# Kernel tuning notes

Measured on AMD Instinct MI355X. Metric: run time of the kernel, lower is better.

Reference implementation:

```python
import jax, jax.numpy as jnp
import numpy as np

B, CH, N = 4, 128, 4096
PC = CH // 2  # pos channels = 64


def setup_inputs() -> dict:
    key = jax.random.key(0)
    ks = jax.random.split(key, 6)
    s_p = 1.0 / np.sqrt(PC)
    s_v = 1.0 / np.sqrt(CH)
    return {
        "pos_bot": jax.random.normal(ks[0], (B, PC, N), dtype=jnp.float32),
        "corr_feats": jax.random.normal(ks[1], (B, CH, N), dtype=jnp.float32),
        "Wp": jax.random.uniform(ks[2], (PC, PC), jnp.float32, -s_p, s_p),
        "bp": jax.random.uniform(ks[3], (PC,), jnp.float32, -s_p, s_p),
        "Wv": jax.random.uniform(ks[4], (CH, CH), jnp.float32, -s_v, s_v),
        "bv": jax.random.uniform(ks[5], (CH,), jnp.float32, -s_v, s_v),
        "beta": jnp.asarray([1.0], dtype=jnp.float32),
    }


def reference(pos_bot, corr_feats, Wp, bp, Wv, bv, beta):
    # 1x1 Conv1d == per-position matmul over channels
    pos = jnp.einsum("oc,bcn->bon", Wp, pos_bot) + bp[None, :, None]      # [B,64,N]
    value = jnp.einsum("oc,bcn->bon", Wv, corr_feats) + bv[None, :, None]  # [B,128,N]

    x = jnp.transpose(pos, (0, 2, 1))  # [B,N,64]
    # squared euclidean pairwise distance: ||xi||^2 + ||xj||^2 - 2 xi.xj
    sq = jnp.sum(x * x, axis=-1)  # [B,N]
    d2 = sq[:, :, None] + sq[:, None, :] - 2.0 * jnp.einsum("bnd,bmd->bnm", x, x)
    d2 = jnp.maximum(d2, 0.0)
    kernel = jnp.exp(-d2 * beta[0])  # [B,N,N] Gaussian RBF

    equation_F = jnp.transpose(value, (0, 2, 1))  # [B,N,128]
    return kernel, equation_F
```

## Files before the change

kernel.cpp:

```cpp
#include <hip/hip_runtime.h>
#include <hip/hip_bf16.h>

typedef _Float16 f16x8 __attribute__((ext_vector_type(8)));
typedef _Float16 f16x4 __attribute__((ext_vector_type(4)));
typedef float    f32x4 __attribute__((ext_vector_type(4)));

constexpr int BB = 4;
constexpr int CH = 128;
constexpr int PC = 64;
constexpr int NN = 4096;

__global__ __launch_bounds__(256) void proj_kernel(
    const float* __restrict__ pos_bot,
    const float* __restrict__ corr,
    const float* __restrict__ Wp,
    const float* __restrict__ bp,
    const float* __restrict__ Wv,
    const float* __restrict__ bv,
    _Float16* __restrict__ xbuf,
    float*    __restrict__ sq,
    float*    __restrict__ eqF)
{
    const int tid  = threadIdx.x;
    const int wid  = tid >> 6;
    const int lane = tid & 63;
    const int l15  = lane & 15;
    const int lg   = lane >> 4;
    const int b    = blockIdx.y & 3;
    const int n    = blockIdx.x * 16 + l15;

    if ((blockIdx.y >> 2) == 0) {
        const int mt = wid;
        f16x8 wf[2], pb[2];
#pragma unroll
        for (int ks = 0; ks < 2; ++ks) {
            const float* wp = Wp + (mt * 16 + l15) * PC + ks * 32 + lg * 8;
            f32x4 w0 = *reinterpret_cast<const f32x4*>(wp);
            f32x4 w1 = *reinterpret_cast<const f32x4*>(wp + 4);
            f16x8 f;
#pragma unroll
            for (int e = 0; e < 4; ++e) { f[e] = (_Float16)w0[e]; f[e + 4] = (_Float16)w1[e]; }
            wf[ks] = f;
            f16x8 g;
#pragma unroll
            for (int e = 0; e < 8; ++e) {
                const int c = ks * 32 + lg * 8 + e;
                g[e] = (_Float16)pos_bot[((size_t)(b * PC + c)) * NN + n];
            }
            pb[ks] = g;
        }

        f32x4 acc = {0.f, 0.f, 0.f, 0.f};
        acc = __builtin_amdgcn_mfma_f32_16x16x32_f16(wf[0], pb[0], acc, 0, 0, 0);
        acc = __builtin_amdgcn_mfma_f32_16x16x32_f16(wf[1], pb[1], acc, 0, 0, 0);

        float partial = 0.f;
        f16x4 h4;
#pragma unroll
        for (int r = 0; r < 4; ++r) {
            const int o = mt * 16 + lg * 4 + r;
            const float v = acc[r] + bp[o];
            const _Float16 h = (_Float16)v;
            h4[r] = h;
            const float hf = (float)h;
            partial = fmaf(hf, hf, partial);
        }
        *reinterpret_cast<f16x4*>(xbuf + ((size_t)(b * NN + n)) * PC + mt * 16 + lg * 4) = h4;

        partial += __shfl_xor(partial, 16);
        partial += __shfl_xor(partial, 32);
        __shared__ float psum[4][16];
        if (lane < 16) psum[wid][l15] = partial;
        __syncthreads();
        if (tid < 16)
            sq[b * NN + blockIdx.x * 16 + tid] =
                psum[0][tid] + psum[1][tid] + psum[2][tid] + psum[3][tid];
        return;
    }

    f16x8 cb[4];
#pragma unroll
    for (int ks = 0; ks < 4; ++ks) {
        f16x8 g;
#pragma unroll
        for (int e = 0; e < 8; ++e) {
            const int c = ks * 32 + lg * 8 + e;
            g[e] = (_Float16)corr[((size_t)(b * CH + c)) * NN + n];
        }
        cb[ks] = g;
    }
#pragma unroll
    for (int half = 0; half < 2; ++half) {
        const int ot = wid + half * 4;
        f32x4 acc = {0.f, 0.f, 0.f, 0.f};
#pragma unroll
        for (int ks = 0; ks < 4; ++ks) {
            const float* wv = Wv + (ot * 16 + l15) * CH + ks * 32 + lg * 8;
            f32x4 w0 = *reinterpret_cast<const f32x4*>(wv);
            f32x4 w1 = *reinterpret_cast<const f32x4*>(wv + 4);
            f16x8 f;
#pragma unroll
            for (int e = 0; e < 4; ++e) { f[e] = (_Float16)w0[e]; f[e + 4] = (_Float16)w1[e]; }
            acc = __builtin_amdgcn_mfma_f32_16x16x32_f16(f, cb[ks], acc, 0, 0, 0);
        }
        f32x4 o4;
#pragma unroll
        for (int r = 0; r < 4; ++r) o4[r] = acc[r] + bv[ot * 16 + lg * 4 + r];
        __builtin_nontemporal_store(
            o4, reinterpret_cast<f32x4*>(eqF + ((size_t)(b * NN + n)) * CH + ot * 16 + lg * 4));
    }
}

__global__ __launch_bounds__(256) void gram_kernel(
    const _Float16* __restrict__ xbuf,
    const float*    __restrict__ sq,
    const float*    __restrict__ beta,
    float*          __restrict__ out)
{
    const int tid  = threadIdx.x;
    const int wid  = tid >> 6;
    const int lane = tid & 63;
    const int l15  = lane & 15;
    const int lg   = lane >> 4;
    const int b    = blockIdx.z;
    const int jb   = blockIdx.x * 512;
    const int rb0  = blockIdx.y * 128;
    const int wjb  = jb + wid * 128;

    const _Float16* xb  = xbuf + (size_t)b * NN * PC;
    const float*    sqb = sq + (size_t)b * NN;

    const float bs   = -beta[0] * 1.44269504088896f;
    const float m2bs = -2.f * bs;

    f16x8 bf[8][2];
    float tj[8];
#pragma unroll
    for (int jtf = 0; jtf < 8; ++jtf) {
        const int j = wjb + jtf * 16 + l15;
#pragma unroll
        for (int ks = 0; ks < 2; ++ks)
            bf[jtf][ks] = *reinterpret_cast<const f16x8*>(
                xb + (size_t)j * PC + ks * 32 + lg * 8);
        tj[jtf] = bs * sqb[j];
    }

    __shared__ float lds[4][16][132];

    for (int rbh = 0; rbh < 2; ++rbh) {
        const int rb = rb0 + rbh * 64;

        for (int sl = 0; sl < 4; ++sl) {
            const int ibase = rb + sl * 16;

            const f16x8 af0 = *reinterpret_cast<const f16x8*>(
                xb + (size_t)(ibase + l15) * PC + lg * 8);
            const f16x8 af1 = *reinterpret_cast<const f16x8*>(
                xb + (size_t)(ibase + l15) * PC + 32 + lg * 8);

            f32x4 acc[8];
#pragma unroll
            for (int jtf = 0; jtf < 8; ++jtf) {
                f32x4 z = {0.f, 0.f, 0.f, 0.f};
                acc[jtf] = __builtin_amdgcn_mfma_f32_16x16x32_f16(af0, bf[jtf][0], z, 0, 0, 0);
            }
#pragma unroll
            for (int jtf = 0; jtf < 8; ++jtf)
                acc[jtf] = __builtin_amdgcn_mfma_f32_16x16x32_f16(af1, bf[jtf][1], acc[jtf], 0, 0, 0);

            const f32x4 sv = *reinterpret_cast<const f32x4*>(sqb + ibase + lg * 4);

#pragma unroll
            for (int jtf = 0; jtf < 8; ++jtf) {
#pragma unroll
                for (int r = 0; r < 4; ++r) {
                    const float ti = bs * sv[r];
                    float arg = fminf(fmaf(m2bs, acc[jtf][r], ti + tj[jtf]), 0.f);
                    lds[wid][lg * 4 + r][jtf * 16 + l15] = __builtin_amdgcn_exp2f(arg);
                }
            }

#pragma unroll
            for (int k = 0; k < 8; ++k) {
                const int row = 2 * k + (lane >> 5);
                const int col = (lane & 31) * 4;
                const f32x4 v = *reinterpret_cast<const f32x4*>(&lds[wid][row][col]);
                __builtin_nontemporal_store(
                    v, reinterpret_cast<f32x4*>(
                           out + ((size_t)(b * NN + ibase + row)) * NN + wjb + col));
            }
        }
    }
}

extern "C" void kernel_launch(void* const* d_in, const int* in_sizes, int n_in,
                              void* d_out, int out_size, void* d_ws, size_t ws_size,
                              hipStream_t stream) {
    const float* pos_bot = (const float*)d_in[0];
    const float* corr    = (const float*)d_in[1];
    const float* Wp      = (const float*)d_in[2];
    const float* bp      = (const float*)d_in[3];
    const float* Wv      = (const float*)d_in[4];
    const float* bv      = (const float*)d_in[5];
    const float* beta    = (const float*)d_in[6];

    float* out = (float*)d_out;
    float* eqF = out + (size_t)BB * NN * NN;

    _Float16* xbuf = (_Float16*)d_ws;
    float* sq = (float*)((char*)d_ws + (size_t)BB * NN * PC * sizeof(_Float16));

    proj_kernel<<<dim3(NN / 16, 2 * BB), 256, 0, stream>>>(
        pos_bot, corr, Wp, bp, Wv, bv, xbuf, sq, eqF);

    gram_kernel<<<dim3(NN / 512, NN / 128, BB), 256, 0, stream>>>(
        xbuf, sq, beta, out);
}
```

Measured before the change: 69.93 us.

## Stage projection inputs through LDS with coalesced loads, widen blocks to 64 positions

The projection kernel now copies a 64-position tile of pos_bot or corr_feats into shared memory with vectorized, coalesced row loads, then builds the f16 MFMA operands from LDS. Previously each lane made strided scalar global loads. Each wave now handles 16 positions across all output tiles instead of one output tile per wave, which removes the cross-wave psum reduction. The cost is more LDS use and a barrier per block, plus four times fewer blocks. The dominant gram kernel is unchanged, so any effect is limited to the smaller projection phase.

```diff
diff --git a/kernel.cpp b/kernel.cpp
--- a/kernel.cpp
+++ b/kernel.cpp
@@ -27,71 +27,91 @@
     const int l15  = lane & 15;
     const int lg   = lane >> 4;
     const int b    = blockIdx.y & 3;
-    const int n    = blockIdx.x * 16 + l15;
-
-    if ((blockIdx.y >> 2) == 0) {
-        const int mt = wid;
-        f16x8 wf[2], pb[2];
+    const int role = blockIdx.y >> 2;
+    const int n0   = blockIdx.x * 64;
+
+    __shared__ float tile[128][68];
+
+    const int nb = wid * 16;
+    const int n  = n0 + nb + l15;
+
+    if (role == 0) {
+        {
+            const int r = tid >> 2, p = tid & 3;
+            const float* src = pos_bot + ((size_t)(b * PC + r)) * NN + n0 + p * 16;
+            float* dst = &tile[r][p * 16];
+#pragma unroll
+            for (int i = 0; i < 4; ++i)
+                *reinterpret_cast<f32x4*>(dst + i * 4) =
+                    *reinterpret_cast<const f32x4*>(src + i * 4);
+        }
+        __syncthreads();
+
+        f16x8 pb[2];
 #pragma unroll
         for (int ks = 0; ks < 2; ++ks) {
-            const float* wp = Wp + (mt * 16 + l15) * PC + ks * 32 + lg * 8;
-            f32x4 w0 = *reinterpret_cast<const f32x4*>(wp);
-            f32x4 w1 = *reinterpret_cast<const f32x4*>(wp + 4);
-            f16x8 f;
-#pragma unroll
-            for (int e = 0; e < 4; ++e) { f[e] = (_Float16)w0[e]; f[e + 4] = (_Float16)w1[e]; }
-            wf[ks] = f;
             f16x8 g;
 #pragma unroll
-            for (int e = 0; e < 8; ++e) {
-                const int c = ks * 32 + lg * 8 + e;
-                g[e] = (_Float16)pos_bot[((size_t)(b * PC + c)) * NN + n];
-            }
+            for (int e = 0; e < 8; ++e)
+                g[e] = (_Float16)tile[ks * 32 + lg * 8 + e][nb + l15];
             pb[ks] = g;
         }
 
-        f32x4 acc = {0.f, 0.f, 0.f, 0.f};
-        acc = __builtin_amdgcn_mfma_f32_16x16x32_f16(wf[0], pb[0], acc, 0, 0, 0);
-        acc = __builtin_amdgcn_mfma_f32_16x16x32_f16(wf[1], pb[1], acc, 0, 0, 0);
-
         float partial = 0.f;
-        f16x4 h4;
-#pragma unroll
-        for (int r = 0; r < 4; ++r) {
-            const int o = mt * 16 + lg * 4 + r;
-            const float v = acc[r] + bp[o];
-            const _Float16 h = (_Float16)v;
-            h4[r] = h;
-            const float hf = (float)h;
-            partial = fmaf(hf, hf, partial);
-        }
-        *reinterpret_cast<f16x4*>(xbuf + ((size_t)(b * NN + n)) * PC + mt * 16 + lg * 4) = h4;
-
+#pragma unroll
+        for (int mt = 0; mt < 4; ++mt) {
+            f32x4 acc = {0.f, 0.f, 0.f, 0.f};
+#pragma unroll
+            for (int ks = 0; ks < 2; ++ks) {
+                const float* wp = Wp + (mt * 16 + l15) * PC + ks * 32 + lg * 8;
+                f32x4 w0 = *reinterpret_cast<const f32x4*>(wp);
+                f32x4 w1 = *reinterpret_cast<const f32x4*>(wp + 4);
+                f16x8 f;
+#pragma unroll
+                for (int e = 0; e < 4; ++e) { f[e] = (_Float16)w0[e]; f[e + 4] = (_Float16)w1[e]; }
+                acc = __builtin_amdgcn_mfma_f32_16x16x32_f16(f, pb[ks], acc, 0, 0, 0);
+            }
+            f16x4 h4;
+#pragma unroll
+            for (int r = 0; r < 4; ++r) {
+                const float v = acc[r] + bp[mt * 16 + lg * 4 + r];
+                const _Float16 h = (_Float16)v;
+                h4[r] = h;
+                const float hf = (float)h;
+                partial = fmaf(hf, hf, partial);
+            }
+            *reinterpret_cast<f16x4*>(xbuf + ((size_t)(b * NN + n)) * PC + mt * 16 + lg * 4) = h4;
+        }
         partial += __shfl_xor(partial, 16);
         partial += __shfl_xor(partial, 32);
-        __shared__ float psum[4][16];
-        if (lane < 16) psum[wid][l15] = partial;
-        __syncthreads();
-        if (tid < 16)
-            sq[b * NN + blockIdx.x * 16 + tid] =
-                psum[0][tid] + psum[1][tid] + psum[2][tid] + psum[3][tid];
+        if (lg == 0) sq[b * NN + n] = partial;
         return;
     }
+
+#pragma unroll
+    for (int u = 0; u < 2; ++u) {
+        const int unit = tid + u * 256;
+        const int r = unit >> 2, p = unit & 3;
+        const float* src = corr + ((size_t)(b * CH + r)) * NN + n0 + p * 16;
+        float* dst = &tile[r][p * 16];
+#pragma unroll
+        for (int i = 0; i < 4; ++i)
+            *reinterpret_cast<f32x4*>(dst + i * 4) =
+                *reinterpret_cast<const f32x4*>(src + i * 4);
+    }
+    __syncthreads();
 
     f16x8 cb[4];
 #pragma unroll
     for (int ks = 0; ks < 4; ++ks) {
         f16x8 g;
 #pragma unroll
-        for (int e = 0; e < 8; ++e) {
-            const int c = ks * 32 + lg * 8 + e;
-            g[e] = (_Float16)corr[((size_t)(b * CH + c)) * NN + n];
-        }
+        for (int e = 0; e < 8; ++e)
+            g[e] = (_Float16)tile[ks * 32 + lg * 8 + e][nb + l15];
         cb[ks] = g;
     }
 #pragma unroll
-    for (int half = 0; half < 2; ++half) {
-        const int ot = wid + half * 4;
+    for (int ot = 0; ot < 8; ++ot) {
         f32x4 acc = {0.f, 0.f, 0.f, 0.f};
 #pragma unroll
         for (int ks = 0; ks < 4; ++ks) {
@@ -210,7 +230,7 @@
     _Float16* xbuf = (_Float16*)d_ws;
     float* sq = (float*)((char*)d_ws + (size_t)BB * NN * PC * sizeof(_Float16));
 
-    proj_kernel<<<dim3(NN / 16, 2 * BB), 256, 0, stream>>>(
+    proj_kernel<<<dim3(NN / 64, 2 * BB), 256, 0, stream>>>(
         pos_bot, corr, Wp, bp, Wv, bv, xbuf, sq, eqF);
 
     gram_kernel<<<dim3(NN / 512, NN / 128, BB), 256, 0, stream>>>(
```

New measurement: 73.48 us. +5.1%, slower.
